# Kernel optimization log

Hardware: AMD Instinct MI355X
Metric: run time of the kernel (lower is better)

The kernel has to match this reference:

```python
import jax, jax.numpy as jnp
import numpy as np

B, N, C = 32, 8192, 512
K = 128          # fixed number of nonzero rows in column `id` per batch (required for torch.stack)
ID = 37          # column index queried


def setup_inputs() -> dict:
    key = jax.random.key(0)
    k1, k2 = jax.random.split(key)
    # random column per row, avoiding ID
    cols = jax.random.randint(k1, (B, N), 0, C - 1)
    cols = jnp.where(cols >= ID, cols + 1, cols)
    # pick exactly K distinct rows per batch to carry column ID
    perm = jnp.argsort(jax.random.uniform(k2, (B, N)), axis=1)  # [B, N] random row permutation
    sel = perm[:, :K]                                           # [B, K] chosen rows
    batch_idx = jnp.arange(B)[:, None]
    cols = cols.at[batch_idx, sel].set(ID)
    one_hot = jax.nn.one_hot(cols, C, dtype=jnp.float32)        # [B, N, C]
    return {"one_hot": one_hot, "id": ID}


def reference(one_hot, id):
    # zeroing column `id` and subtracting leaves only column `id`; summing over
    # the column dim therefore just extracts one_hot[:, :, id].
    col = one_hot[:, :, id]                       # [B, N]
    block_id = col[:, :, None, None]              # [B, N, 1, 1] == stack(...).unsqueeze(-1)
    # nonzero row indices per batch, ascending, fixed count K (stable sort puts
    # nonzero rows first while preserving ascending row order)
    mask_key = (col == 0).astype(jnp.int32)       # 0 for nonzero rows, 1 otherwise
    indices = jnp.argsort(mask_key, axis=1, stable=True)[:, :K]  # [B, K]
    return block_id, indices
```

## Files before the change

kernel.cpp:

```cpp
#include <hip/hip_runtime.h>
#include <hip/hip_bf16.h>

#define PB 32
#define PN 8192
#define PC 512
#define PK 128


__global__ __launch_bounds__(256) void gather_col(
    const float* __restrict__ one_hot,
    const int* __restrict__ id_ptr,
    float* __restrict__ out0)
{
    int i = blockIdx.x * 256 + threadIdx.x;
    int id = id_ptr[0];
    out0[i] = one_hot[(size_t)i * PC + (size_t)id];
}

__global__ __launch_bounds__(1024) void compact_idx(
    const float* __restrict__ out0,
    float* __restrict__ out1)
{
    const int b    = blockIdx.x;
    const int tid  = threadIdx.x;
    const int wave = tid >> 6;
    const int lane = tid & 63;

    __shared__ unsigned int wave_cnt[16];

    const float* row = out0 + (size_t)b * PN;

    float vals[8];
#pragma unroll
    for (int p = 0; p < 8; ++p)
        vals[p] = row[p * 1024 + tid];

    unsigned int running = 0;
#pragma unroll
    for (int p = 0; p < 8; ++p) {
        const bool pred = (vals[p] != 0.0f);
        const unsigned long long mask = __ballot(pred);
        if (lane == 0) wave_cnt[wave] = (unsigned int)__popcll(mask);
        __syncthreads();

        unsigned int prefix = 0, total = 0;
#pragma unroll
        for (int w = 0; w < 16; ++w) {
            unsigned int c = wave_cnt[w];
            total += c;
            if (w < wave) prefix += c;
        }

        if (pred) {
            unsigned int rank = (unsigned int)__popcll(mask & ((1ULL << lane) - 1ULL));
            unsigned int pos  = running + prefix + rank;
            if (pos < PK) {
                out1[b * PK + pos] = (float)(p * 1024 + tid);
            }
        }
        running += total;
        __syncthreads();
    }
}

extern "C" void kernel_launch(void* const* d_in, const int* in_sizes, int n_in,
                              void* d_out, int out_size, void* d_ws, size_t ws_size,
                              hipStream_t stream) {
    const float* one_hot = nullptr;
    const int* id_ptr = nullptr;
    for (int i = 0; i < n_in; ++i) {
        if (in_sizes[i] == 1) id_ptr = (const int*)d_in[i];
        else                  one_hot = (const float*)d_in[i];
    }

    float* out0 = (float*)d_out;
    float* out1 = (float*)d_out + (size_t)PB * PN;

    gather_col<<<dim3((PB * PN) / 256), dim3(256), 0, stream>>>(one_hot, id_ptr, out0);
    compact_idx<<<dim3(PB), dim3(1024), 0, stream>>>(out0, out1);
}
```

Baseline: 575.3 us.

## Fuse column gather and index compaction into one kernel with cross-block handoff

Merges the gather kernel and the per-batch compaction kernel into one launch of 256 blocks. Each block gathers one 1024-row chunk, compacts its nonzero indices into a workspace slot, and publishes the count with a release-tagged atomic. The last chunk block of each batch spins on the other chunks' tags and writes the final 128 indices. This removes a kernel launch and the re-read of out0, and uses nontemporal loads and stores for the strided gather. It depends on spin-waiting between co-resident blocks and on workspace tags that could still be stale from a previous call, since the slots are not reset between calls.

```diff
diff --git a/kernel.cpp b/kernel.cpp
--- a/kernel.cpp
+++ b/kernel.cpp
@@ -1,65 +1,93 @@
 #include <hip/hip_runtime.h>
-#include <hip/hip_bf16.h>
 
 #define PB 32
 #define PN 8192
 #define PC 512
 #define PK 128
+#define CHUNK 1024
+#define NCHUNK 8
+#define SLOT_STRIDE 256
+#define TAG 0x40000000u
 
 
-__global__ __launch_bounds__(256) void gather_col(
+__global__ __launch_bounds__(1024) void fused_filter(
     const float* __restrict__ one_hot,
     const int* __restrict__ id_ptr,
-    float* __restrict__ out0)
+    float* __restrict__ out0,
+    float* __restrict__ out1,
+    unsigned int* __restrict__ ws)
 {
-    int i = blockIdx.x * 256 + threadIdx.x;
-    int id = id_ptr[0];
-    out0[i] = one_hot[(size_t)i * PC + (size_t)id];
-}
-
-__global__ __launch_bounds__(1024) void compact_idx(
-    const float* __restrict__ out0,
-    float* __restrict__ out1)
-{
-    const int b    = blockIdx.x;
+    const int g    = blockIdx.x;
+    const int b    = g >> 3;
+    const int c    = g & 7;
     const int tid  = threadIdx.x;
     const int wave = tid >> 6;
     const int lane = tid & 63;
+    const int n    = c * CHUNK + tid;
+    const int i    = b * PN + n;
 
     __shared__ unsigned int wave_cnt[16];
+    __shared__ unsigned int m_cnt[NCHUNK];
 
-    const float* row = out0 + (size_t)b * PN;
+    const int id = id_ptr[0];
 
-    float vals[8];
+    float v = __builtin_nontemporal_load(one_hot + (size_t)i * PC + (size_t)id);
+    __builtin_nontemporal_store(v, out0 + i);
+
+    const bool pred = (v != 0.0f);
+    const unsigned long long mask = __ballot(pred);
+    if (lane == 0) wave_cnt[wave] = (unsigned int)__popcll(mask);
+    __syncthreads();
+
+    unsigned int prefix = 0, total = 0;
 #pragma unroll
-    for (int p = 0; p < 8; ++p)
-        vals[p] = row[p * 1024 + tid];
+    for (int w = 0; w < 16; ++w) {
+        unsigned int cc = wave_cnt[w];
+        if (w < wave) prefix += cc;
+        total += cc;
+    }
 
-    unsigned int running = 0;
+    unsigned int* slot = ws + (size_t)g * SLOT_STRIDE;
+    if (pred) {
+        unsigned int rank = (unsigned int)__popcll(mask & ((1ULL << lane) - 1ULL));
+        slot[1 + prefix + rank] = (unsigned int)n;
+    }
+    __syncthreads();
+    __threadfence();
+    if (tid == 0)
+        __hip_atomic_store(&slot[0], TAG | total,
+                           __ATOMIC_RELEASE, __HIP_MEMORY_SCOPE_AGENT);
+
+    if (c != 7) return;
+
+    unsigned int* base = ws + (size_t)(b * NCHUNK) * SLOT_STRIDE;
+    if (tid < NCHUNK) {
+        unsigned int tagv;
+        if (tid == 7) {
+            tagv = TAG | total;
+        } else {
+            unsigned int* s = base + tid * SLOT_STRIDE;
+            do {
+                tagv = __hip_atomic_load(s, __ATOMIC_ACQUIRE,
+                                         __HIP_MEMORY_SCOPE_AGENT);
+            } while ((tagv & 0xFFFF0000u) != TAG);
+        }
+        m_cnt[tid] = tagv & 0xFFFFu;
+    }
+    __syncthreads();
+
+    if (tid < PK) {
+        unsigned int p = 0, off = 0;
+        int j = 0;
 #pragma unroll
-    for (int p = 0; p < 8; ++p) {
-        const bool pred = (vals[p] != 0.0f);
-        const unsigned long long mask = __ballot(pred);
-        if (lane == 0) wave_cnt[wave] = (unsigned int)__popcll(mask);
-        __syncthreads();
-
-        unsigned int prefix = 0, total = 0;
-#pragma unroll
-        for (int w = 0; w < 16; ++w) {
-            unsigned int c = wave_cnt[w];
-            total += c;
-            if (w < wave) prefix += c;
+        for (int q = 0; q < NCHUNK; ++q) {
+            unsigned int cq = m_cnt[q];
+            if ((unsigned)tid >= p && (unsigned)tid < p + cq) { j = q; off = tid - p; }
+            p += cq;
         }
-
-        if (pred) {
-            unsigned int rank = (unsigned int)__popcll(mask & ((1ULL << lane) - 1ULL));
-            unsigned int pos  = running + prefix + rank;
-            if (pos < PK) {
-                out1[b * PK + pos] = (float)(p * 1024 + tid);
-            }
-        }
-        running += total;
-        __syncthreads();
+        unsigned int idx = base[j * SLOT_STRIDE + 1 + off];
+        float val = ((unsigned)tid < p) ? (float)idx : 0.0f;
+        out1[b * PK + tid] = val;
     }
 }
 
@@ -76,6 +104,6 @@
     float* out0 = (float*)d_out;
     float* out1 = (float*)d_out + (size_t)PB * PN;
 
-    gather_col<<<dim3((PB * PN) / 256), dim3(256), 0, stream>>>(one_hot, id_ptr, out0);
-    compact_idx<<<dim3(PB), dim3(1024), 0, stream>>>(out0, out1);
+    fused_filter<<<dim3(PB * NCHUNK), dim3(1024), 0, stream>>>(
+        one_hot, id_ptr, out0, out1, (unsigned int*)d_ws);
 }
```

Result: slower. 629.3 us (+9.4%).
